# Optimization experiments

Hardware: AMD Instinct MI355X
Metric: run time of the kernel (lower is better)

The kernel has to match this reference:

```python
import jax, jax.numpy as jnp
import numpy as np

B, C, L = 16, 64, 512
L_P = 16
D_MODEL = 1024
STRIDE = 8
N_P = (L - L_P) // STRIDE + 2  # 64 patches
PERIOD = L // 2                # statsmodels period = series_input_length / 2


def setup_inputs() -> dict:
    key = jax.random.key(0)
    ks = jax.random.split(key, 11)
    s = 0.02  # small init scale for weights
    return {
        "data_x": jax.random.normal(ks[0], (B, C, L), jnp.float32),
        "gamma": jax.random.uniform(ks[1], (B, C, L), jnp.float32),
        "beta": jax.random.uniform(ks[2], (B, C, L), jnp.float32),
        "w_trend": jax.random.normal(ks[3], (L_P, L), jnp.float32) * s,
        "b_trend": jax.random.normal(ks[4], (L_P,), jnp.float32) * s,
        "w_seasonal": jax.random.normal(ks[5], (L_P, L), jnp.float32) * s,
        "b_seasonal": jax.random.normal(ks[6], (L_P,), jnp.float32) * s,
        "w_resid": jax.random.normal(ks[7], (L_P, L), jnp.float32) * s,
        "b_resid": jax.random.normal(ks[8], (L_P,), jnp.float32) * s,
        "w_g": jax.random.normal(ks[9], (D_MODEL, 3 * L_P), jnp.float32) * s,
        "b_g": jax.random.normal(ks[10], (D_MODEL,), jnp.float32) * s,
    }


def _decompose(x):
    """Vectorized statsmodels seasonal_decompose(model='additive', period=L//2).

    trend: centered moving average with filter [0.5,1,...,1,0.5]/p (even period),
           NaN edges -> replaced by 0 (as in the torch module).
    seasonal: per-phase nanmean of detrended, demeaned, tiled to length L.
    resid: detrended - seasonal on the valid (non-NaN) region, 0 elsewhere.
    x: [B, C, L] -> (trend, seasonal, resid) each [B, C, L].
    """
    p = PERIOD
    filt = jnp.concatenate([jnp.full((1,), 0.5, x.dtype),
                            jnp.ones((p - 1,), x.dtype),
                            jnp.full((1,), 0.5, x.dtype)]) / p  # len p+1 (p even)
    head = p // 2               # leading NaN count (filter is symmetric)
    nvalid = L - p              # valid trend samples
    xf = x.reshape(B * C, 1, L)
    tv = jax.lax.conv_general_dilated(xf, filt.reshape(1, 1, p + 1),
                                      (1,), "VALID")[:, 0, :]  # [BC, L-p]
    trend = jnp.zeros((B * C, L), x.dtype).at[:, head:head + nvalid].set(tv)
    dv = x.reshape(B * C, L)[:, head:head + nvalid] - tv  # detrended, valid region
    # per-phase nanmean over valid detrended samples
    phase = (head + jnp.arange(nvalid)) % p               # phase of each valid index
    sums = jnp.zeros((B * C, p), x.dtype).at[:, phase].add(dv)
    counts = jnp.zeros((p,), x.dtype).at[phase].add(1.0)
    pa = sums / counts                                    # period averages [BC, p]
    pa = pa - jnp.mean(pa, axis=1, keepdims=True)
    seasonal = jnp.tile(pa, (1, L // p))                  # L = 2p exactly
    resid = jnp.zeros((B * C, L), x.dtype).at[:, head:head + nvalid].set(
        dv - seasonal[:, head:head + nvalid])
    return (trend.reshape(B, C, L), seasonal.reshape(B, C, L),
            resid.reshape(B, C, L))


def reference(data_x, gamma, beta, w_trend, b_trend, w_seasonal, b_seasonal,
              w_resid, b_resid, w_g, b_g):
    # 'transformed': per-channel stats (dim=1), torch var is unbiased (ddof=1), epsi=0
    mean = jnp.mean(data_x, axis=1)
    var = jnp.var(data_x, axis=1, ddof=1)
    mean = (mean / jnp.sqrt(var))[:, None, :]             # [B,1,L] broadcast over C
    x = gamma * (data_x - mean) + beta
    x = jax.lax.stop_gradient(x)                          # season() detaches
    trend, seasonal, resid = _decompose(x)
    t = trend @ w_trend.T + b_trend                       # [B,C,L_p]
    s = seasonal @ w_seasonal.T + b_seasonal
    r = resid @ w_resid.T + b_resid
    feats = jnp.concatenate([t, s, r], axis=-1)           # [B,C,3*L_p]
    feats = jnp.broadcast_to(feats[:, :, None, :], (B, C, N_P, 3 * L_P))
    return feats @ w_g.T + b_g                            # [B,C,N_p,D_MODEL]
```

## Files before the change

kernel.cpp:

```cpp
#include <hip/hip_runtime.h>
#include <math.h>

#define BB   16
#define CC   64
#define LL   512
#define LP   16
#define DM   1024
#define NP   64
#define PRD  256
#define HEAD 128
#define NV   256

typedef float f32x4 __attribute__((ext_vector_type(4)));

#define OFF_MEANP 0
#define OFF_WSF   8192
#define OFF_WRS   12288
#define OFF_WGT   12304
#define OFF_FEATS (12304 + 49152)

__global__ __launch_bounds__(256) void statsprep_kernel(
    const float* __restrict__ dx, const float* __restrict__ w_s,
    const float* __restrict__ w_r, const float* __restrict__ w_g,
    float* __restrict__ ws)
{
    const int tid = threadIdx.x, bid = blockIdx.x;
    if (bid < 32) {
        int id = bid * 256 + tid;
        int b = id >> 9, l = id & 511;
        const float* p = dx + (size_t)b * CC * LL + l;
        float s = 0.f, sq = 0.f;
#pragma unroll 8
        for (int c = 0; c < CC; ++c) {
            float v = p[(size_t)c * LL];
            s += v; sq += v * v;
        }
        float mean = s * (1.0f / CC);
        float var  = (sq - (float)CC * mean * mean) * (1.0f / (CC - 1));
        ws[OFF_MEANP + id] = mean / sqrtf(var);
    } else if (bid == 32) {
#pragma unroll
        for (int idx = tid; idx < 16 * PRD; idx += 256) {
            int g = idx >> 8, m = idx & 255;
            ws[OFF_WSF + idx] = w_s[g * LL + m] + w_s[g * LL + PRD + m];
        }
        int g = tid >> 4, ln = tid & 15;
        float s = 0.f;
        for (int k = ln; k < PRD; k += 16) s += w_r[g * LL + HEAD + k];
#pragma unroll
        for (int m = 8; m; m >>= 1) s += __shfl_xor(s, m, 16);
        if (ln == 0) ws[OFF_WRS + g] = s;
    } else {
        int base = (bid - 33) * 3072 + tid;
#pragma unroll
        for (int k = 0; k < 12; ++k) {
            int e = base + k * 256;
            int j = e >> 10, d = e & 1023;
            ws[OFF_WGT + e] = w_g[d * 48 + j];
        }
    }
}

__global__ __launch_bounds__(256) void feats_kernel(
    const float* __restrict__ dx,    const float* __restrict__ gamma,
    const float* __restrict__ beta,  const float* __restrict__ w_t,
    const float* __restrict__ b_t,   const float* __restrict__ b_s,
    const float* __restrict__ b_r,   float* __restrict__ ws)
{
    __shared__ __align__(16) float xs[LL];
    __shared__ __align__(16) float pps[LL/2 + 1];
    __shared__ __align__(16) float tvs[NV];
    __shared__ __align__(16) float pas[PRD];
    __shared__ __align__(16) float feats[48];
    __shared__ float wsum[4];
    __shared__ float wred[4];

    const int tid  = threadIdx.x;
    const int lane = tid & 63;
    const int wv   = tid >> 6;
    const int bc   = blockIdx.x;
    const int b    = bc >> 6;

    const size_t base = (size_t)bc * LL;
    float2 xv = ((const float2*)(dx    + base))[tid];
    float2 gv = ((const float2*)(gamma + base))[tid];
    float2 bv = ((const float2*)(beta  + base))[tid];
    float2 mv = ((const float2*)(ws + OFF_MEANP + (size_t)b * LL))[tid];
    float2 xp;
    xp.x = gv.x * (xv.x - mv.x) + bv.x;
    xp.y = gv.y * (xv.y - mv.y) + bv.y;
    ((float2*)xs)[tid] = xp;

    float v = xp.x + xp.y;
#pragma unroll
    for (int d = 1; d < 64; d <<= 1) {
        float t = __shfl_up(v, d, 64);
        if (lane >= d) v += t;
    }
    if (lane == 63) wsum[wv] = v;
    __syncthreads();
    float off = 0.f;
    for (int w = 0; w < wv; ++w) off += wsum[w];
    pps[tid + 1] = v + off;
    if (tid == 0) pps[0] = 0.f;
    __syncthreads();

    const int i  = tid;
    const int k2 = i + 257;
    const float Pi = pps[i  >> 1] + ((i  & 1) ? xs[i  & ~1] : 0.f);
    const float Pk = pps[k2 >> 1] + ((k2 & 1) ? xs[k2 & ~1] : 0.f);
    const float tv = (Pk - Pi - 0.5f * (xs[i] + xs[i + 256])) * (1.0f / 256.0f);
    tvs[i] = tv;
    const float dv = xs[HEAD + i] - tv;

    float r = dv;
#pragma unroll
    for (int m = 32; m; m >>= 1) r += __shfl_xor(r, m, 64);
    if (lane == 0) wred[wv] = r;
    __syncthreads();
    const float mdv = (wred[0] + wred[1] + wred[2] + wred[3]) * (1.0f / 256.0f);

    pas[(i + 128) & 255] = dv - mdv;
    __syncthreads();

    {
        const int g  = tid >> 4;
        const int ln = tid & 15;
        const f32x4* wt4  = (const f32x4*)(w_t + g * LL + HEAD);
        const f32x4* wsf4 = (const f32x4*)(ws + OFF_WSF + g * PRD);
        const f32x4* tv4  = (const f32x4*)tvs;
        const f32x4* pa4  = (const f32x4*)pas;
        float at = 0.f, as = 0.f;
#pragma unroll
        for (int q = 0; q < 4; ++q) {
            const int m = ln * 4 + q;
            f32x4 t = tv4[m], p = pa4[m];
            f32x4 a = wt4[m], sfw = wsf4[m];
            at += t.x * a.x + t.y * a.y + t.z * a.z + t.w * a.w;
            as += p.x * sfw.x + p.y * sfw.y + p.z * sfw.z + p.w * sfw.w;
        }
#pragma unroll
        for (int msk = 8; msk; msk >>= 1) {
            at += __shfl_xor(at, msk, 64);
            as += __shfl_xor(as, msk, 64);
        }
        if (ln == 0) {
            feats[g]      = at + b_t[g];
            feats[16 + g] = as + b_s[g];
            feats[32 + g] = mdv * ws[OFF_WRS + g] + b_r[g];
        }
    }
    __syncthreads();

    if (tid < 12)
        ((f32x4*)(ws + OFF_FEATS))[bc * 12 + tid] = ((const f32x4*)feats)[tid];
}

__global__ __launch_bounds__(256) void mvbcast_kernel(
    const float* __restrict__ ws, const float* __restrict__ b_g,
    float* __restrict__ out)
{
    __shared__ float sf[48];
    __shared__ __align__(16) float sres[256];

    const int tid = threadIdx.x;
    const int bc  = blockIdx.x >> 2;
    const int q   = blockIdx.x & 3;

    if (tid < 48) sf[tid] = ws[OFF_FEATS + bc * 48 + tid];
    __syncthreads();

    const int d = q * 256 + tid;
    const float* wT = ws + OFF_WGT + d;
    float acc = b_g[d];
#pragma unroll
    for (int j = 0; j < 48; ++j)
        acc = fmaf(sf[j], wT[j * 1024], acc);
    sres[tid] = acc;
    __syncthreads();

    const int lane = tid & 63;
    const int wv   = tid >> 6;
    const f32x4 v = ((const f32x4*)sres)[lane];
    f32x4* op = (f32x4*)out + (size_t)bc * (NP * DM / 4)
              + (size_t)wv * (DM / 4) + q * 64 + lane;
#pragma unroll
    for (int k = 0; k < 16; ++k)
        op[(size_t)k * 4 * (DM / 4)] = v;
}

extern "C" void kernel_launch(void* const* d_in, const int* in_sizes, int n_in,
                              void* d_out, int out_size, void* d_ws, size_t ws_size,
                              hipStream_t stream) {
    const float* dx    = (const float*)d_in[0];
    const float* gamma = (const float*)d_in[1];
    const float* beta  = (const float*)d_in[2];
    const float* w_t   = (const float*)d_in[3];
    const float* b_t   = (const float*)d_in[4];
    const float* w_s   = (const float*)d_in[5];
    const float* b_s   = (const float*)d_in[6];
    const float* w_r   = (const float*)d_in[7];
    const float* b_r   = (const float*)d_in[8];
    const float* w_g   = (const float*)d_in[9];
    const float* b_g   = (const float*)d_in[10];
    float* out = (float*)d_out;
    float* ws  = (float*)d_ws;

    statsprep_kernel<<<49, 256, 0, stream>>>(dx, w_s, w_r, w_g, ws);
    feats_kernel<<<BB * CC, 256, 0, stream>>>(
        dx, gamma, beta, w_t, b_t, b_s, b_r, ws);
    mvbcast_kernel<<<BB * CC * 4, 256, 0, stream>>>(ws, b_g, out);
}
```

Baseline: 75.45 us.

## Fuse feature computation with projection and broadcast into one kernel

Merges the per-row feature kernel and the projection/broadcast kernel into a single kernel, so each block computes its 48 features, projects them to all 1024 outputs, and writes the 64 broadcast copies itself. This removes a kernel launch and the workspace round trip for the features. In exchange the grid drops from 4096 to 1024 blocks, each doing four times the projection and store work, which may lower the parallelism available for the large output write.

```diff
diff --git a/kernel.cpp b/kernel.cpp
--- a/kernel.cpp
+++ b/kernel.cpp
@@ -17,7 +17,6 @@
 #define OFF_WSF   8192
 #define OFF_WRS   12288
 #define OFF_WGT   12304
-#define OFF_FEATS (12304 + 49152)
 
 __global__ __launch_bounds__(256) void statsprep_kernel(
     const float* __restrict__ dx, const float* __restrict__ w_s,
@@ -61,17 +60,19 @@
     }
 }
 
-__global__ __launch_bounds__(256) void feats_kernel(
+__global__ __launch_bounds__(256) void fused_kernel(
     const float* __restrict__ dx,    const float* __restrict__ gamma,
     const float* __restrict__ beta,  const float* __restrict__ w_t,
     const float* __restrict__ b_t,   const float* __restrict__ b_s,
-    const float* __restrict__ b_r,   float* __restrict__ ws)
+    const float* __restrict__ b_r,   const float* __restrict__ b_g,
+    const float* __restrict__ ws,    float* __restrict__ out)
 {
     __shared__ __align__(16) float xs[LL];
     __shared__ __align__(16) float pps[LL/2 + 1];
     __shared__ __align__(16) float tvs[NV];
     __shared__ __align__(16) float pas[PRD];
     __shared__ __align__(16) float feats[48];
+    __shared__ __align__(16) float sres[DM];
     __shared__ float wsum[4];
     __shared__ float wred[4];
 
@@ -152,41 +153,31 @@
     }
     __syncthreads();
 
-    if (tid < 12)
-        ((f32x4*)(ws + OFF_FEATS))[bc * 12 + tid] = ((const f32x4*)feats)[tid];
-}
-
-__global__ __launch_bounds__(256) void mvbcast_kernel(
-    const float* __restrict__ ws, const float* __restrict__ b_g,
-    float* __restrict__ out)
-{
-    __shared__ float sf[48];
-    __shared__ __align__(16) float sres[256];
-
-    const int tid = threadIdx.x;
-    const int bc  = blockIdx.x >> 2;
-    const int q   = blockIdx.x & 3;
-
-    if (tid < 48) sf[tid] = ws[OFF_FEATS + bc * 48 + tid];
-    __syncthreads();
-
-    const int d = q * 256 + tid;
-    const float* wT = ws + OFF_WGT + d;
-    float acc = b_g[d];
-#pragma unroll
-    for (int j = 0; j < 48; ++j)
-        acc = fmaf(sf[j], wT[j * 1024], acc);
-    sres[tid] = acc;
-    __syncthreads();
-
-    const int lane = tid & 63;
-    const int wv   = tid >> 6;
-    const f32x4 v = ((const f32x4*)sres)[lane];
-    f32x4* op = (f32x4*)out + (size_t)bc * (NP * DM / 4)
-              + (size_t)wv * (DM / 4) + q * 64 + lane;
-#pragma unroll
-    for (int k = 0; k < 16; ++k)
-        op[(size_t)k * 4 * (DM / 4)] = v;
+    const float* wT = ws + OFF_WGT;
+    float acc0 = b_g[tid];
+    float acc1 = b_g[256 + tid];
+    float acc2 = b_g[512 + tid];
+    float acc3 = b_g[768 + tid];
+#pragma unroll
+    for (int j = 0; j < 48; ++j) {
+        const float fj = feats[j];
+        const float* w = wT + j * DM + tid;
+        acc0 = fmaf(fj, w[0],   acc0);
+        acc1 = fmaf(fj, w[256], acc1);
+        acc2 = fmaf(fj, w[512], acc2);
+        acc3 = fmaf(fj, w[768], acc3);
+    }
+    sres[tid]       = acc0;
+    sres[256 + tid] = acc1;
+    sres[512 + tid] = acc2;
+    sres[768 + tid] = acc3;
+    __syncthreads();
+
+    const f32x4 res = ((const f32x4*)sres)[tid];
+    f32x4* op = (f32x4*)out + (size_t)bc * (NP * DM / 4) + tid;
+#pragma unroll
+    for (int n = 0; n < NP; ++n)
+        op[(size_t)n * (DM / 4)] = res;
 }
 
 extern "C" void kernel_launch(void* const* d_in, const int* in_sizes, int n_in,
@@ -207,7 +198,6 @@
     float* ws  = (float*)d_ws;
 
     statsprep_kernel<<<49, 256, 0, stream>>>(dx, w_s, w_r, w_g, ws);
-    feats_kernel<<<BB * CC, 256, 0, stream>>>(
-        dx, gamma, beta, w_t, b_t, b_s, b_r, ws);
-    mvbcast_kernel<<<BB * CC * 4, 256, 0, stream>>>(ws, b_g, out);
+    fused_kernel<<<BB * CC, 256, 0, stream>>>(
+        dx, gamma, beta, w_t, b_t, b_s, b_r, b_g, ws, out);
 }
```

Measured after the change: 66.08 us. 12.4% less time.
